# Kernel optimization log

Measured on AMD Instinct MI355X. Metric: run time of the kernel, lower is better.

The kernel has to match this reference:

```python
import jax, jax.numpy as jnp
import numpy as np

SEQ_LEN = 512
JOINT_DIM = 96
DECAY = 0.8


def _predefined_weights(n: int, decay: float) -> np.ndarray:
    # W[i, j] = decay**(i-j) for j <= i, each row normalized to sum 1.
    i = np.arange(n)[:, None]
    j = np.arange(n)[None, :]
    lower = j <= i
    exponent = np.where(lower, i - j, 0)
    w = np.where(lower, decay ** exponent.astype(np.float64), 0.0)
    row_sum = w.sum(axis=1, keepdims=True)
    w = np.where(row_sum > 0, w / row_sum, w)
    return w.astype(np.float32)


def setup_inputs() -> dict:
    key = jax.random.key(0)
    kx, ko = jax.random.split(key)
    x = jax.random.normal(kx, (64, SEQ_LEN, JOINT_DIM), dtype=jnp.float32)
    # learnable parameter (initialized to zeros in the module; small noise for generality)
    learnable_offset = 0.02 * jax.random.normal(ko, (JOINT_DIM, SEQ_LEN, SEQ_LEN), dtype=jnp.float32)
    predefined_weights = jnp.asarray(_predefined_weights(SEQ_LEN, DECAY))
    return {"x": x, "learnable_offset": learnable_offset, "predefined_weights": predefined_weights}


def reference(x, learnable_offset, predefined_weights):
    # masks[j] = softmax(predefined + offset[j], axis=-1)   -> [J, N, N]
    masks = jax.nn.softmax(predefined_weights[None, :, :] + learnable_offset, axis=-1)
    # out[b, n, j] = sum_m masks[j, n, m] * x[b, m, j]      -> [B, N, J]
    return jnp.einsum('jnm,bmj->bnj', masks, x)
```

## Files before the change

kernel.cpp:

```cpp
#include <hip/hip_runtime.h>

#define BATCH 64
#define SEQ   512
#define JDIM  96
#define TN    64
#define KC    64
#define NCH   (SEQ / KC)
#define LDB   72

typedef __attribute__((ext_vector_type(8))) short bf16x8;
typedef __attribute__((ext_vector_type(4))) float f32x4;

#define LOG2D (-0.32192809489f)

__device__ __forceinline__ unsigned short f2bf(float f) {
  unsigned u = __float_as_uint(f);
  u += 0x7FFFu + ((u >> 16) & 1u);
  return (unsigned short)(u >> 16);
}

__global__ __launch_bounds__(256) void transpose_in_kernel(
    const float* __restrict__ x, unsigned short* __restrict__ xT) {
  __shared__ float tile[JDIM * 65];
  const int r0 = blockIdx.x * 64;
  const int R = BATCH * SEQ;
  for (int idx = threadIdx.x; idx < 64 * 24; idx += 256) {
    int rr = idx / 24, jg = idx - rr * 24;
    float4 v = *(const float4*)(x + (size_t)(r0 + rr) * JDIM + 4 * jg);
    tile[(4 * jg + 0) * 65 + rr] = v.x;
    tile[(4 * jg + 1) * 65 + rr] = v.y;
    tile[(4 * jg + 2) * 65 + rr] = v.z;
    tile[(4 * jg + 3) * 65 + rr] = v.w;
  }
  __syncthreads();
  for (int idx = threadIdx.x; idx < JDIM * 8; idx += 256) {
    int jj = idx >> 3, rg = idx & 7;
    const float* t = &tile[jj * 65 + 8 * rg];
    uint4 pk;
    pk.x = (unsigned)f2bf(t[0]) | ((unsigned)f2bf(t[1]) << 16);
    pk.y = (unsigned)f2bf(t[2]) | ((unsigned)f2bf(t[3]) << 16);
    pk.z = (unsigned)f2bf(t[4]) | ((unsigned)f2bf(t[5]) << 16);
    pk.w = (unsigned)f2bf(t[6]) | ((unsigned)f2bf(t[7]) << 16);
    *(uint4*)(&xT[(size_t)jj * R + r0 + 8 * rg]) = pk;
  }
}

__global__ __launch_bounds__(256, 3) void fused_kernel(
    const unsigned short* __restrict__ xT,
    const float* __restrict__ off,
    float* __restrict__ outT) {
  __shared__ unsigned short As[BATCH * LDB];
  __shared__ unsigned short Bs[TN * LDB];
  __shared__ float Lred[TN * 17];
  __shared__ float Linv[TN];

  const int j  = blockIdx.x >> 3;
  const int n0 = (blockIdx.x & 7) * TN;

  const int tid  = threadIdx.x;
  const int lane = tid & 63;
  const int wid  = tid >> 6;
  const int ln   = lane & 15;
  const int quad = lane >> 4;
  const int bw   = (wid & 1) * 32;
  const int nw   = (wid >> 1) * 32;

  f32x4 acc[2][2];
#pragma unroll
  for (int i = 0; i < 2; ++i)
#pragma unroll
    for (int q = 0; q < 2; ++q) acc[i][q] = (f32x4){0.f, 0.f, 0.f, 0.f};
  float Lpart[4] = {0.f, 0.f, 0.f, 0.f};

  const unsigned short* xTj = xT + (size_t)j * (BATCH * SEQ);
  const float* offj = off + (size_t)j * (SEQ * SEQ);

  const int a_kg = tid & 7;
  const int a_b  = tid >> 3;
  const int b_mg = tid & 15;
  const int b_n  = tid >> 4;

  float cn[4];
#pragma unroll
  for (int p = 0; p < 4; ++p) {
    const int n = n0 + b_n + 16 * p;
    cn[p] = 0.2f / (1.0f - exp2f(LOG2D * (float)(n + 1)));
  }

  for (int ch = 0; ch < NCH; ++ch) {
    const int m0 = ch * KC;
#pragma unroll
    for (int p = 0; p < 2; ++p) {
      const int b = a_b + 32 * p;
      uint4 v = *(const uint4*)(xTj + (size_t)b * SEQ + m0 + 8 * a_kg);
      *(uint4*)(&As[b * LDB + 8 * a_kg]) = v;
    }
    const int mbase = m0 + 4 * b_mg;
#pragma unroll
    for (int p = 0; p < 4; ++p) {
      const int nl = b_n + 16 * p;
      const int n  = n0 + nl;
      const float4 o = *(const float4*)(offj + (size_t)n * SEQ + mbase);
      const float c = cn[p];
      const float d0 = (float)(n - mbase);
      const float p0 = (d0 >= 0.f) ? c * exp2f(LOG2D * d0) : 0.f;
      const float p1 = (d0 >= 1.f) ? c * exp2f(LOG2D * (d0 - 1.f)) : 0.f;
      const float p2 = (d0 >= 2.f) ? c * exp2f(LOG2D * (d0 - 2.f)) : 0.f;
      const float p3 = (d0 >= 3.f) ? c * exp2f(LOG2D * (d0 - 3.f)) : 0.f;
      const float e0 = __expf(o.x + p0);
      const float e1 = __expf(o.y + p1);
      const float e2 = __expf(o.z + p2);
      const float e3 = __expf(o.w + p3);
      Lpart[p] += (e0 + e1) + (e2 + e3);
      uint2 pk;
      pk.x = (unsigned)f2bf(e0) | ((unsigned)f2bf(e1) << 16);
      pk.y = (unsigned)f2bf(e2) | ((unsigned)f2bf(e3) << 16);
      *(uint2*)(&Bs[nl * LDB + 4 * b_mg]) = pk;
    }
    __syncthreads();
#pragma unroll
    for (int ks = 0; ks < KC; ks += 32) {
      bf16x8 afrag[2], bfrag[2];
#pragma unroll
      for (int i = 0; i < 2; ++i)
        afrag[i] = *(const bf16x8*)(&As[(bw + 16 * i + ln) * LDB + ks + 8 * quad]);
#pragma unroll
      for (int q = 0; q < 2; ++q)
        bfrag[q] = *(const bf16x8*)(&Bs[(nw + 16 * q + ln) * LDB + ks + 8 * quad]);
#pragma unroll
      for (int i = 0; i < 2; ++i)
#pragma unroll
        for (int q = 0; q < 2; ++q)
          acc[i][q] = __builtin_amdgcn_mfma_f32_16x16x32_bf16(afrag[i], bfrag[q], acc[i][q], 0, 0, 0);
    }
    __syncthreads();
  }

#pragma unroll
  for (int p = 0; p < 4; ++p) Lred[(b_n + 16 * p) * 17 + b_mg] = Lpart[p];
  __syncthreads();
  if (tid < TN) {
    float s = 0.f;
#pragma unroll
    for (int i = 0; i < 16; ++i) s += Lred[tid * 17 + i];
    Linv[tid] = 1.0f / s;
  }
  __syncthreads();

  float* outTj = outT + (size_t)j * (SEQ * BATCH);
#pragma unroll
  for (int q = 0; q < 2; ++q) {
    const int nc = nw + 16 * q + ln;
    const float linv = Linv[nc];
#pragma unroll
    for (int i = 0; i < 2; ++i) {
      float4 v;
      v.x = acc[i][q][0] * linv;
      v.y = acc[i][q][1] * linv;
      v.z = acc[i][q][2] * linv;
      v.w = acc[i][q][3] * linv;
      *(float4*)(&outTj[(size_t)(n0 + nc) * BATCH + bw + 16 * i + 4 * quad]) = v;
    }
  }
}

__global__ __launch_bounds__(256) void transpose_out_kernel(
    const float* __restrict__ outT, float* __restrict__ out) {
  __shared__ float tile[JDIM * 65];
  const int n = blockIdx.x;
  for (int idx = threadIdx.x; idx < JDIM * 16; idx += 256) {
    int jj = idx >> 4, g = idx & 15;
    float4 v = *(const float4*)(outT + ((size_t)jj * SEQ + n) * BATCH + 4 * g);
    float* t = &tile[jj * 65 + 4 * g];
    t[0] = v.x; t[1] = v.y; t[2] = v.z; t[3] = v.w;
  }
  __syncthreads();
  for (int idx = threadIdx.x; idx < BATCH * 24; idx += 256) {
    int b = idx / 24, jg = idx - b * 24;
    float4 w;
    w.x = tile[(4 * jg + 0) * 65 + b];
    w.y = tile[(4 * jg + 1) * 65 + b];
    w.z = tile[(4 * jg + 2) * 65 + b];
    w.w = tile[(4 * jg + 3) * 65 + b];
    *(float4*)(out + ((size_t)b * SEQ + n) * JDIM + 4 * jg) = w;
  }
}

extern "C" void kernel_launch(void* const* d_in, const int* in_sizes, int n_in,
                              void* d_out, int out_size, void* d_ws, size_t ws_size,
                              hipStream_t stream) {
  const float* x   = (const float*)d_in[0];
  const float* off = (const float*)d_in[1];
  float* out = (float*)d_out;

  unsigned short* xT = (unsigned short*)d_ws;
  float* outT = (float*)((char*)d_ws + (size_t)JDIM * BATCH * SEQ * sizeof(unsigned short));

  transpose_in_kernel<<<BATCH * SEQ / 64, 256, 0, stream>>>(x, xT);
  fused_kernel<<<JDIM * (SEQ / TN), 256, 0, stream>>>(xT, off, outT);
  transpose_out_kernel<<<SEQ, 256, 0, stream>>>(outT, out);
}
```

Before: 173.2 us.

## Double-buffer LDS tiles and prefetch offset/x chunks into registers

Double-buffers the A and B shared-memory tiles and prefetches the next chunk's global loads into registers two chunks ahead. The exp/bf16 staging of chunk ch+1 now overlaps the MFMA of chunk ch, and one barrier per chunk is removed. It also replaces three exp2f calls per element group with multiplications of a single base value by decay powers, which cuts transcendental work. In exchange it doubles LDS use and raises register pressure, which may reduce occupancy under the 3-blocks launch bound.

```diff
diff --git a/kernel.cpp b/kernel.cpp
--- a/kernel.cpp
+++ b/kernel.cpp
@@ -49,8 +49,8 @@
     const unsigned short* __restrict__ xT,
     const float* __restrict__ off,
     float* __restrict__ outT) {
-  __shared__ unsigned short As[BATCH * LDB];
-  __shared__ unsigned short Bs[TN * LDB];
+  __shared__ unsigned short As[2][BATCH * LDB];
+  __shared__ unsigned short Bs[2][TN * LDB];
   __shared__ float Lred[TN * 17];
   __shared__ float Linv[TN];
 
@@ -87,54 +87,78 @@
     cn[p] = 0.2f / (1.0f - exp2f(LOG2D * (float)(n + 1)));
   }
 
+  uint4  va[2];
+  float4 vo[4];
+
+#define LOADCH(CH) do {                                                          \
+    const int m0_ = (CH) * KC;                                                   \
+    va[0] = *(const uint4*)(xTj + (size_t)a_b * SEQ + m0_ + 8 * a_kg);           \
+    va[1] = *(const uint4*)(xTj + (size_t)(a_b + 32) * SEQ + m0_ + 8 * a_kg);    \
+    _Pragma("unroll")                                                            \
+    for (int p = 0; p < 4; ++p)                                                  \
+      vo[p] = *(const float4*)(offj + (size_t)(n0 + b_n + 16 * p) * SEQ + m0_ + 4 * b_mg); \
+  } while (0)
+
+#define STAGECH(BUF, CH) do {                                                    \
+    const int m0_ = (CH) * KC;                                                   \
+    *(uint4*)(&As[BUF][a_b * LDB + 8 * a_kg]) = va[0];                           \
+    *(uint4*)(&As[BUF][(a_b + 32) * LDB + 8 * a_kg]) = va[1];                    \
+    const int mbase = m0_ + 4 * b_mg;                                            \
+    _Pragma("unroll")                                                            \
+    for (int p = 0; p < 4; ++p) {                                                \
+      const int nl = b_n + 16 * p;                                               \
+      const int n  = n0 + nl;                                                    \
+      const float4 o = vo[p];                                                    \
+      const float cc = cn[p];                                                    \
+      const float d0 = (float)(n - mbase);                                       \
+       \
+      const float pb = cc * exp2f(LOG2D * d0);                                   \
+      const float p0 = (d0 >= 0.f) ? pb : 0.f;                                   \
+      const float p1 = (d0 >= 1.f) ? pb * 1.25f : 0.f;                           \
+      const float p2 = (d0 >= 2.f) ? pb * 1.5625f : 0.f;                         \
+      const float p3 = (d0 >= 3.f) ? pb * 1.953125f : 0.f;                       \
+      const float e0 = __expf(o.x + p0);                                         \
+      const float e1 = __expf(o.y + p1);                                         \
+      const float e2 = __expf(o.z + p2);                                         \
+      const float e3 = __expf(o.w + p3);                                         \
+      Lpart[p] += (e0 + e1) + (e2 + e3);                                         \
+      uint2 pk;                                                                  \
+      pk.x = (unsigned)f2bf(e0) | ((unsigned)f2bf(e1) << 16);                    \
+      pk.y = (unsigned)f2bf(e2) | ((unsigned)f2bf(e3) << 16);                    \
+      *(uint2*)(&Bs[BUF][nl * LDB + 4 * b_mg]) = pk;                             \
+    }                                                                            \
+  } while (0)
+
+  LOADCH(0);
+  STAGECH(0, 0);
+  LOADCH(1);
+  __syncthreads();
+
+  int c = 0;
+#pragma unroll
   for (int ch = 0; ch < NCH; ++ch) {
-    const int m0 = ch * KC;
-#pragma unroll
-    for (int p = 0; p < 2; ++p) {
-      const int b = a_b + 32 * p;
-      uint4 v = *(const uint4*)(xTj + (size_t)b * SEQ + m0 + 8 * a_kg);
-      *(uint4*)(&As[b * LDB + 8 * a_kg]) = v;
-    }
-    const int mbase = m0 + 4 * b_mg;
-#pragma unroll
-    for (int p = 0; p < 4; ++p) {
-      const int nl = b_n + 16 * p;
-      const int n  = n0 + nl;
-      const float4 o = *(const float4*)(offj + (size_t)n * SEQ + mbase);
-      const float c = cn[p];
-      const float d0 = (float)(n - mbase);
-      const float p0 = (d0 >= 0.f) ? c * exp2f(LOG2D * d0) : 0.f;
-      const float p1 = (d0 >= 1.f) ? c * exp2f(LOG2D * (d0 - 1.f)) : 0.f;
-      const float p2 = (d0 >= 2.f) ? c * exp2f(LOG2D * (d0 - 2.f)) : 0.f;
-      const float p3 = (d0 >= 3.f) ? c * exp2f(LOG2D * (d0 - 3.f)) : 0.f;
-      const float e0 = __expf(o.x + p0);
-      const float e1 = __expf(o.y + p1);
-      const float e2 = __expf(o.z + p2);
-      const float e3 = __expf(o.w + p3);
-      Lpart[p] += (e0 + e1) + (e2 + e3);
-      uint2 pk;
-      pk.x = (unsigned)f2bf(e0) | ((unsigned)f2bf(e1) << 16);
-      pk.y = (unsigned)f2bf(e2) | ((unsigned)f2bf(e3) << 16);
-      *(uint2*)(&Bs[nl * LDB + 4 * b_mg]) = pk;
-    }
-    __syncthreads();
 #pragma unroll
     for (int ks = 0; ks < KC; ks += 32) {
       bf16x8 afrag[2], bfrag[2];
 #pragma unroll
       for (int i = 0; i < 2; ++i)
-        afrag[i] = *(const bf16x8*)(&As[(bw + 16 * i + ln) * LDB + ks + 8 * quad]);
+        afrag[i] = *(const bf16x8*)(&As[c][(bw + 16 * i + ln) * LDB + ks + 8 * quad]);
 #pragma unroll
       for (int q = 0; q < 2; ++q)
-        bfrag[q] = *(const bf16x8*)(&Bs[(nw + 16 * q + ln) * LDB + ks + 8 * quad]);
+        bfrag[q] = *(const bf16x8*)(&Bs[c][(nw + 16 * q + ln) * LDB + ks + 8 * quad]);
 #pragma unroll
       for (int i = 0; i < 2; ++i)
 #pragma unroll
         for (int q = 0; q < 2; ++q)
           acc[i][q] = __builtin_amdgcn_mfma_f32_16x16x32_bf16(afrag[i], bfrag[q], acc[i][q], 0, 0, 0);
     }
+    if (ch + 1 < NCH) STAGECH(c ^ 1, ch + 1);
+    if (ch + 2 < NCH) LOADCH(ch + 2);
     __syncthreads();
-  }
+    c ^= 1;
+  }
+#undef LOADCH
+#undef STAGECH
 
 #pragma unroll
   for (int p = 0; p < 4; ++p) Lred[(b_n + 16 * p) * 17 + b_mg] = Lpart[p];
```

Result: slower. 178.9 us (+3.3%).
